# Kernel optimization log

Hardware: AMD Instinct MI355X
Metric: run time of the kernel (lower is better)

Reference implementation:

```python
import jax, jax.numpy as jnp
import numpy as np
from jax import lax

B, C, H, W = 2, 256, 64, 64
OUT_C = 256
D_QK = C // 16   # 16
D_V = C // 2     # 128
BN_EPS = 1e-5


def setup_inputs() -> dict:
    key = jax.random.key(0)
    ks = jax.random.split(key, 10)
    s = lambda fan: 1.0 / np.sqrt(fan)
    return {
        "input1": jax.random.normal(ks[0], (B, C, H, W), jnp.float32),
        "input2": jax.random.normal(ks[1], (B, C, H, W), jnp.float32),
        "Wq": jax.random.normal(ks[2], (D_QK, C), jnp.float32) * s(C),
        "bq": jnp.zeros((D_QK,), jnp.float32),
        "Wk": jax.random.normal(ks[3], (D_QK, C), jnp.float32) * s(C),
        "bk": jnp.zeros((D_QK,), jnp.float32),
        "Wv": jax.random.normal(ks[4], (D_V, C), jnp.float32) * s(C),
        "bv": jnp.zeros((D_V,), jnp.float32),
        "gamma": jnp.array(0.5, jnp.float32),  # nn.Parameter(zeros(1)); nonzero to exercise the path
        "Wcat": jax.random.normal(ks[5], (OUT_C, C, 3, 3), jnp.float32) * s(C * 9),
        "bn_gamma": jnp.ones((OUT_C,), jnp.float32),
        "bn_beta": jnp.zeros((OUT_C,), jnp.float32),
    }


def _conv1x1(x, Wt, b):
    # x: (B,C,H,W), Wt: (O,C) -> (B,O,H,W)
    return jnp.einsum('bchw,oc->bohw', x, Wt) + b[None, :, None, None]


def _branch(x_self, x_other, Wq, bq, Wk, bk, Wv, bv, gamma):
    N = H * W
    q = _conv1x1(x_self, Wq, bq).reshape(B, D_QK, N)   # q of self
    k = _conv1x1(x_other, Wk, bk).reshape(B, D_QK, N)  # k of other
    v = _conv1x1(x_self, Wv, bv).reshape(B, D_V, N)    # v of self
    # attn[b,n,m] = softmax_m( q[:,n] . k[:,m] / sqrt(d) )
    attn = jax.nn.softmax(jnp.einsum('bdn,bdm->bnm', q, k) / jnp.sqrt(jnp.float32(D_QK)), axis=-1)
    out = jnp.einsum('bcm,bnm->bcn', v, attn).reshape(B, D_V, H, W)  # v @ attn^T
    out = jnp.concatenate([out, x_self[:, :C // 2]], axis=1)  # (B,C,H,W)
    return gamma * out + x_self


def reference(input1, input2, Wq, bq, Wk, bk, Wv, bv, gamma, Wcat, bn_gamma, bn_beta):
    out1 = _branch(input1, input2, Wq, bq, Wk, bk, Wv, bv, gamma)
    out2 = _branch(input2, input1, Wq, bq, Wk, bk, Wv, bv, gamma)
    s = out1 + out2
    y = lax.conv_general_dilated(s, Wcat, (1, 1), 'SAME',
                                 dimension_numbers=('NCHW', 'OIHW', 'NCHW'))
    # BatchNorm (inference: running_mean=0, running_var=1)
    inv = 1.0 / jnp.sqrt(1.0 + BN_EPS)
    y = y * (bn_gamma * inv)[None, :, None, None] + bn_beta[None, :, None, None]
    feat_sum = jax.nn.relu(y)
    return (feat_sum, out1, out2)
```

## Files before the change

kernel.cpp:

```cpp
#include <hip/hip_runtime.h>

#define N_PIX 4096
#define CCH 256
#define DV 128

typedef __attribute__((ext_vector_type(8))) short bf16x8;
typedef __attribute__((ext_vector_type(4))) float f32x4;
typedef __attribute__((ext_vector_type(8))) short short8;

__device__ __forceinline__ short f2bf(float f) {
    unsigned u = __builtin_bit_cast(unsigned, f);
    u += 0x7fffu + ((u >> 16) & 1u);
    return (short)(u >> 16);
}

__global__ __launch_bounds__(512) void qkv_kernel(
    const float* __restrict__ x1, const float* __restrict__ x2,
    const short* __restrict__ wqkv,
    const float* __restrict__ bq, const float* __restrict__ bk,
    const float* __restrict__ bv,
    short* __restrict__ qb, short* __restrict__ kb, short* __restrict__ vb)
{
    __shared__ short xT[64][68];

    const int tid = threadIdx.x;
    const int lane = tid & 63;
    const int w = tid >> 6;
    const int g = lane >> 4, l15 = lane & 15;
    const int n0 = blockIdx.x * 64;
    const int ib = blockIdx.y;
    const int i = ib >> 1, b = ib & 1;
    const float* x = (i == 0 ? x1 : x2) + (size_t)b * CCH * N_PIX;

    const int px2 = tid & 31, c4 = tid >> 5;

    const int rhalf = (w >> 2) * 80;

    f32x4 acc[5];
    #pragma unroll
    for (int jl = 0; jl < 5; ++jl) {
        int rbase = rhalf + jl * 16;
        float bias;
        if (rbase == 0)       bias = bq[l15];
        else if (rbase == 16) bias = bk[l15];
        else                  bias = bv[rbase - 32 + l15];
        acc[jl] = (f32x4){bias, bias, bias, bias};
    }

    float2 xr[4];
    {
        #pragma unroll
        for (int jj = 0; jj < 4; ++jj)
            xr[jj] = *(const float2*)&x[(size_t)(c4 * 4 + jj) * N_PIX + n0 + px2 * 2];
    }

    for (int ci = 0; ci < 4; ++ci) {
        __syncthreads();
        {
            short4 w0, w1;
            w0.x = f2bf(xr[0].x); w0.y = f2bf(xr[1].x); w0.z = f2bf(xr[2].x); w0.w = f2bf(xr[3].x);
            w1.x = f2bf(xr[0].y); w1.y = f2bf(xr[1].y); w1.z = f2bf(xr[2].y); w1.w = f2bf(xr[3].y);
            *(short4*)&xT[px2 * 2 + 0][c4 * 4] = w0;
            *(short4*)&xT[px2 * 2 + 1][c4 * 4] = w1;
        }
        __syncthreads();
        if (ci < 3) {
            #pragma unroll
            for (int jj = 0; jj < 4; ++jj)
                xr[jj] = *(const float2*)
                    &x[(size_t)((ci + 1) * 64 + c4 * 4 + jj) * N_PIX + n0 + px2 * 2];
        }
        bf16x8 a0 = *(const bf16x8*)&xT[(w & 3) * 16 + l15][g * 8];
        bf16x8 a1 = *(const bf16x8*)&xT[(w & 3) * 16 + l15][32 + g * 8];
        #pragma unroll
        for (int jl = 0; jl < 5; ++jl) {
            int rbase = rhalf + jl * 16;
            const short* wrow = wqkv + (size_t)(rbase + l15) * CCH + ci * 64;
            bf16x8 b0 = *(const bf16x8*)&wrow[g * 8];
            bf16x8 b1 = *(const bf16x8*)&wrow[32 + g * 8];
            acc[jl] = __builtin_amdgcn_mfma_f32_16x16x32_bf16(a0, b0, acc[jl], 0, 0, 0);
            acc[jl] = __builtin_amdgcn_mfma_f32_16x16x32_bf16(a1, b1, acc[jl], 0, 0, 0);
        }
    }

    const int px_base = n0 + (w & 3) * 16 + g * 4;
    #pragma unroll
    for (int jl = 0; jl < 5; ++jl) {
        int rbase = rhalf + jl * 16;
        if (rbase == 0) {
            #pragma unroll
            for (int rr = 0; rr < 4; ++rr)
                qb[((size_t)ib * N_PIX + px_base + rr) * 16 + l15] = f2bf(acc[jl][rr]);
        } else if (rbase == 16) {
            #pragma unroll
            for (int rr = 0; rr < 4; ++rr)
                kb[((size_t)ib * N_PIX + px_base + rr) * 16 + l15] = f2bf(acc[jl][rr]);
        } else {
            int c = rbase - 32 + l15;
            short4 s;
            s.x = f2bf(acc[jl][0]); s.y = f2bf(acc[jl][1]);
            s.z = f2bf(acc[jl][2]); s.w = f2bf(acc[jl][3]);
            *(short4*)&vb[((size_t)ib * DV + c) * N_PIX + px_base] = s;
        }
    }
}

__global__ __launch_bounds__(256, 4) void attn_kernel(
    const short* __restrict__ qg, const short* __restrict__ kg,
    const short* __restrict__ vg,
    float* __restrict__ out1, float* __restrict__ out2,
    float* __restrict__ featf, float* __restrict__ lpart)
{
    __shared__ short k_lds[64 * 24];
    __shared__ short p_lds[64 * 72];

    const int tid = threadIdx.x;
    const int lane = tid & 63;
    const int w = tid >> 6;
    const int gk = lane >> 4;
    const int l15 = lane & 15;

    const int B_ = blockIdx.x;
    const int pm = B_ & 7;
    const int pb = pm >> 1, mh = pm & 1;
    const int nt = B_ >> 3;
    const int n0 = nt * 64;
    const int br = pb >> 1, b = pb & 1;

    const short* qp = qg + (size_t)pb * N_PIX * 16;
    const short* kp = kg + (size_t)((br ^ 1) * 2 + b) * N_PIX * 16 + (size_t)(mh * 2048) * 16;
    const short* vp = vg + (size_t)pb * DV * N_PIX + mh * 2048;

    bf16x8 aq = {};
    if (lane < 32)
        aq = *(const bf16x8*)&qp[(size_t)(n0 + w * 16 + l15) * 16 + gk * 8];

    f32x4 acc[2][4];
    #pragma unroll
    for (int cc = 0; cc < 2; ++cc)
        #pragma unroll
        for (int nb = 0; nb < 4; ++nb) acc[cc][nb] = (f32x4){0.f, 0.f, 0.f, 0.f};
    float lsum[4] = {0.f, 0.f, 0.f, 0.f};

    const short* vbase = vp + (size_t)(w * 32 + l15) * N_PIX + gk * 8;
    const int krow = tid - 192;

    int4 vbuf0[4], vbuf1[4];
    int4 kr0 = {}, kr1 = {};

    {
        #pragma unroll
        for (int cc = 0; cc < 2; ++cc)
            #pragma unroll
            for (int m2 = 0; m2 < 2; ++m2)
                vbuf0[cc * 2 + m2] = *(const int4*)&vbase[(size_t)cc * 16 * N_PIX + m2 * 32];
        if (tid >= 192) {
            kr0 = *(const int4*)&kp[(size_t)krow * 16];
            kr1 = *(const int4*)&kp[(size_t)krow * 16 + 8];
            *(int4*)&k_lds[krow * 24] = kr0;
            *(int4*)&k_lds[krow * 24 + 8] = kr1;
        }
        __syncthreads();
    }

    for (int t0 = 0; t0 < 32; t0 += 2) {
        #pragma unroll
        for (int half = 0; half < 2; ++half) {
            const int t = t0 + half;
            int4* vcur = half ? vbuf1 : vbuf0;
            int4* vnxt = half ? vbuf0 : vbuf1;
            if (t + 1 < 32) {
                #pragma unroll
                for (int cc = 0; cc < 2; ++cc)
                    #pragma unroll
                    for (int m2 = 0; m2 < 2; ++m2)
                        vnxt[cc * 2 + m2] = *(const int4*)
                            &vbase[(size_t)cc * 16 * N_PIX + (t + 1) * 64 + m2 * 32];
                if (tid >= 192) {
                    kr0 = *(const int4*)&kp[(size_t)((t + 1) * 64 + krow) * 16];
                    kr1 = *(const int4*)&kp[(size_t)((t + 1) * 64 + krow) * 16 + 8];
                }
            }
            #pragma unroll
            for (int h = 0; h < 4; ++h) {
                bf16x8 bk_ = {};
                if (lane < 32)
                    bk_ = *(const bf16x8*)&k_lds[(h * 16 + l15) * 24 + gk * 8];
                f32x4 s = __builtin_amdgcn_mfma_f32_16x16x32_bf16(
                    aq, bk_, (f32x4){0.f, 0.f, 0.f, 0.f}, 0, 0, 0);
                #pragma unroll
                for (int rr = 0; rr < 4; ++rr) {
                    float e = __expf(s[rr] * 0.25f);
                    lsum[rr] += e;
                    unsigned u = __builtin_bit_cast(unsigned, e);
                    p_lds[(w * 16 + gk * 4 + rr) * 72 + h * 16 + l15] = (short)(u >> 16);
                }
            }
            __syncthreads();
            if (t + 1 < 32 && tid >= 192) {
                *(int4*)&k_lds[krow * 24] = kr0;
                *(int4*)&k_lds[krow * 24 + 8] = kr1;
            }
            __builtin_amdgcn_s_setprio(1);
            #pragma unroll
            for (int m2 = 0; m2 < 2; ++m2) {
                #pragma unroll
                for (int nb = 0; nb < 4; ++nb) {
                    bf16x8 bp = *(const bf16x8*)&p_lds[(nb * 16 + l15) * 72 + m2 * 32 + gk * 8];
                    #pragma unroll
                    for (int cc = 0; cc < 2; ++cc) {
                        bf16x8 av = __builtin_bit_cast(bf16x8, vcur[cc * 2 + m2]);
                        acc[cc][nb] = __builtin_amdgcn_mfma_f32_16x16x32_bf16(
                            av, bp, acc[cc][nb], 0, 0, 0);
                    }
                }
            }
            __builtin_amdgcn_s_setprio(0);
            __syncthreads();
        }
    }

    #pragma unroll
    for (int rr = 0; rr < 4; ++rr) {
        float v = lsum[rr];
        v += __shfl_xor(v, 1); v += __shfl_xor(v, 2);
        v += __shfl_xor(v, 4); v += __shfl_xor(v, 8);
        lsum[rr] = v;
    }
    if (l15 == 0) {
        #pragma unroll
        for (int rr = 0; rr < 4; ++rr)
            lpart[(size_t)(pb * 2 + mh) * N_PIX + n0 + w * 16 + gk * 4 + rr] = lsum[rr];
    }

    if (mh == 0) {
        float* Od = (br ? out2 : out1) + (size_t)b * CCH * N_PIX;
        #pragma unroll
        for (int cc = 0; cc < 2; ++cc)
            #pragma unroll
            for (int nb = 0; nb < 4; ++nb)
                #pragma unroll
                for (int rr = 0; rr < 4; ++rr) {
                    int c = w * 32 + cc * 16 + gk * 4 + rr;
                    Od[(size_t)c * N_PIX + n0 + nb * 16 + l15] = acc[cc][nb][rr];
                }
    } else {
        float* Ps = featf + (size_t)(pb * 64 + nt) * (128 * 64);
        #pragma unroll
        for (int cc = 0; cc < 2; ++cc)
            #pragma unroll
            for (int nb = 0; nb < 4; ++nb)
                #pragma unroll
                for (int rr = 0; rr < 4; ++rr) {
                    int c = w * 32 + cc * 16 + gk * 4 + rr;
                    Ps[c * 64 + nb * 16 + l15] = acc[cc][nb][rr];
                }
    }
}

__global__ __launch_bounds__(256) void merge_kernel(
    const float* __restrict__ x1, const float* __restrict__ x2,
    const float* __restrict__ featf, const float* __restrict__ lpart,
    const float* __restrict__ gamma_p,
    float* __restrict__ out1, float* __restrict__ out2,
    short* __restrict__ s_t)
{
    __shared__ short st[32 * 264];
    __shared__ float rls[2][32];
    const int tid = threadIdx.x;
    const int px0 = blockIdx.x * 32;
    const int b = blockIdx.y;
    const int nt = blockIdx.x >> 1;
    const int q32 = (blockIdx.x & 1) * 32;
    const float* xa_ = x1 + (size_t)b * CCH * N_PIX;
    const float* xb_ = x2 + (size_t)b * CCH * N_PIX;
    float* o1 = out1 + (size_t)b * CCH * N_PIX;
    float* o2 = out2 + (size_t)b * CCH * N_PIX;
    const float* T1 = featf + (size_t)(b * 64 + nt) * (128 * 64);
    const float* T2 = featf + (size_t)((2 + b) * 64 + nt) * (128 * 64);

    if (tid < 64) {
        int h = tid >> 5, j = tid & 31;
        int pbh = h ? (2 + b) : b;
        float l = lpart[(size_t)(pbh * 2 + 0) * N_PIX + px0 + j]
                + lpart[(size_t)(pbh * 2 + 1) * N_PIX + px0 + j];
        rls[h][j] = 1.0f / l;
    }
    __syncthreads();
    const float gmm = gamma_p[0];

    for (int idx = tid; idx < 2048; idx += 256) {
        int c = idx >> 3, p4 = idx & 7;
        size_t off = (size_t)c * N_PIX + px0 + p4 * 4;
        float4 va = *(const float4*)&xa_[off];
        float4 vb2 = *(const float4*)&xb_[off];
        float4 r1, r2;
        if (c < 128) {
            float4 pa = *(const float4*)&o1[off];
            float4 pc = *(const float4*)&o2[off];
            float4 a1 = *(const float4*)&T1[c * 64 + q32 + p4 * 4];
            float4 c1 = *(const float4*)&T2[c * 64 + q32 + p4 * 4];
            r1.x = gmm * (pa.x + a1.x) * rls[0][p4 * 4 + 0] + va.x;
            r1.y = gmm * (pa.y + a1.y) * rls[0][p4 * 4 + 1] + va.y;
            r1.z = gmm * (pa.z + a1.z) * rls[0][p4 * 4 + 2] + va.z;
            r1.w = gmm * (pa.w + a1.w) * rls[0][p4 * 4 + 3] + va.w;
            r2.x = gmm * (pc.x + c1.x) * rls[1][p4 * 4 + 0] + vb2.x;
            r2.y = gmm * (pc.y + c1.y) * rls[1][p4 * 4 + 1] + vb2.y;
            r2.z = gmm * (pc.z + c1.z) * rls[1][p4 * 4 + 2] + vb2.z;
            r2.w = gmm * (pc.w + c1.w) * rls[1][p4 * 4 + 3] + vb2.w;
        } else {
            size_t offl = (size_t)(c - 128) * N_PIX + px0 + p4 * 4;
            float4 val = *(const float4*)&xa_[offl];
            float4 vbl = *(const float4*)&xb_[offl];
            r1.x = gmm * val.x + va.x; r1.y = gmm * val.y + va.y;
            r1.z = gmm * val.z + va.z; r1.w = gmm * val.w + va.w;
            r2.x = gmm * vbl.x + vb2.x; r2.y = gmm * vbl.y + vb2.y;
            r2.z = gmm * vbl.z + vb2.z; r2.w = gmm * vbl.w + vb2.w;
        }
        *(float4*)&o1[off] = r1;
        *(float4*)&o2[off] = r2;
        st[(p4 * 4 + 0) * 264 + c] = f2bf(r1.x + r2.x);
        st[(p4 * 4 + 1) * 264 + c] = f2bf(r1.y + r2.y);
        st[(p4 * 4 + 2) * 264 + c] = f2bf(r1.z + r2.z);
        st[(p4 * 4 + 3) * 264 + c] = f2bf(r1.w + r2.w);
    }
    __syncthreads();
    for (int idx = tid; idx < 1024; idx += 256) {
        int px = idx >> 5, seg = idx & 31;
        int4 v = *(const int4*)&st[px * 264 + seg * 8];
        *(int4*)&s_t[((size_t)b * N_PIX + px0 + px) * CCH + seg * 8] = v;
    }
}

__global__ __launch_bounds__(256) void prep_w(
    const float* __restrict__ Wcat,
    const float* __restrict__ Wq, const float* __restrict__ Wk,
    const float* __restrict__ Wv,
    short* __restrict__ wfmt, short* __restrict__ wqkv)
{
    if (blockIdx.x < 288) {
        int idx = blockIdx.x * 256 + threadIdx.x;
        int lane = idx & 63;
        int ocg = (idx >> 6) & 15;
        int chunk = (idx >> 10) & 7;
        int tap = idx >> 13;
        int oc = ocg * 16 + (lane & 15);
        int ic0 = chunk * 32 + (lane >> 4) * 8;
        short8 v;
        #pragma unroll
        for (int j = 0; j < 8; ++j)
            v[j] = f2bf(Wcat[((size_t)oc * CCH + ic0 + j) * 9 + tap]);
        *(short8*)&wfmt[(size_t)idx * 8] = v;
    } else {
        int idx = (blockIdx.x - 288) * 1024 + threadIdx.x * 4;
        int r = idx >> 8, c = idx & 255;
        const float* src;
        if (r < 16)      src = Wq + (size_t)r * CCH + c;
        else if (r < 32) src = Wk + (size_t)(r - 16) * CCH + c;
        else             src = Wv + (size_t)(r - 32) * CCH + c;
        float4 f = *(const float4*)src;
        short4 s;
        s.x = f2bf(f.x); s.y = f2bf(f.y); s.z = f2bf(f.z); s.w = f2bf(f.w);
        *(short4*)&wqkv[idx] = s;
    }
}

__global__ __launch_bounds__(256) void conv_mfma(
    const short* __restrict__ s_t, const short* __restrict__ wfmt,
    const float* __restrict__ bn_gamma, const float* __restrict__ bn_beta,
    float* __restrict__ feat)
{
    __shared__ short s_lds[264 * 40];
    const int tid = threadIdx.x;
    const int lane = tid & 63;
    const int wv = tid >> 6;
    const int g = lane >> 4, l15 = lane & 15;

    const int bx = blockIdx.x;
    const int oc_t = bx & 3;
    const int pt = bx >> 2;
    const int b = pt >> 5;
    const int h0 = (pt & 31) * 2;

    f32x4 acc[2][4] = {};

    const short* sbase = s_t + (size_t)b * N_PIX * CCH;
    const short* wf = wfmt + ((size_t)(oc_t * 4) * 64 + lane) * 8;

    for (int ci = 0; ci < 8; ++ci) {
        const int ic0 = ci * 32;
        __syncthreads();
        for (int idx = tid; idx < 1056; idx += 256) {
            int seg = idx & 3, pos = idx >> 2;
            int row = pos / 66, wi = pos - row * 66;
            int hr = h0 - 1 + row, w = wi - 1;
            int4 val = {0, 0, 0, 0};
            if (hr >= 0 && hr < 64 && (unsigned)w < 64u)
                val = *(const int4*)&sbase[((size_t)(hr * 64 + w)) * CCH + ic0 + seg * 8];
            *(int4*)&s_lds[pos * 40 + seg * 8] = val;
        }
        __syncthreads();

        const short* wfc = wf + (size_t)ci * 8192;
        bf16x8 a0[4], a1[4];
        #pragma unroll
        for (int j = 0; j < 4; ++j) a0[j] = *(const bf16x8*)&wfc[j * 512];

        for (int tap = 0; tap < 9; ++tap) {
            bf16x8* ac = (tap & 1) ? a1 : a0;
            bf16x8* an = (tap & 1) ? a0 : a1;
            if (tap < 8) {
                const short* wfn = wfc + (size_t)(tap + 1) * 65536;
                #pragma unroll
                for (int j = 0; j < 4; ++j) an[j] = *(const bf16x8*)&wfn[j * 512];
            }
            int ky = (tap >= 6) ? 2 : (tap >= 3 ? 1 : 0);
            int kx = tap - ky * 3;
            #pragma unroll
            for (int f = 0; f < 2; ++f) {
                int fr = wv * 2 + f;
                int rl = fr >> 2, wc0 = (fr & 3) * 16;
                bf16x8 bb = *(const bf16x8*)
                    &s_lds[((rl + ky) * 66 + wc0 + l15 + kx) * 40 + g * 8];
                #pragma unroll
                for (int j = 0; j < 4; ++j)
                    acc[f][j] = __builtin_amdgcn_mfma_f32_16x16x32_bf16(
                        ac[j], bb, acc[f][j], 0, 0, 0);
            }
        }
    }

    const float inv = rsqrtf(1.0f + 1e-5f);
    #pragma unroll
    for (int f = 0; f < 2; ++f) {
        int fr = wv * 2 + f;
        int rl = fr >> 2, wc0 = (fr & 3) * 16;
        int h = h0 + rl, wcol = wc0 + l15;
        #pragma unroll
        for (int j = 0; j < 4; ++j) {
            #pragma unroll
            for (int r = 0; r < 4; ++r) {
                int oc = oc_t * 64 + j * 16 + g * 4 + r;
                float y = acc[f][j][r] * (bn_gamma[oc] * inv) + bn_beta[oc];
                feat[((size_t)b * CCH + oc) * N_PIX + h * 64 + wcol] = fmaxf(y, 0.f);
            }
        }
    }
}

extern "C" void kernel_launch(void* const* d_in, const int* in_sizes, int n_in,
                              void* d_out, int out_size, void* d_ws, size_t ws_size,
                              hipStream_t stream) {
    const float* x1    = (const float*)d_in[0];
    const float* x2    = (const float*)d_in[1];
    const float* Wq    = (const float*)d_in[2];
    const float* bq    = (const float*)d_in[3];
    const float* Wk    = (const float*)d_in[4];
    const float* bk    = (const float*)d_in[5];
    const float* Wv    = (const float*)d_in[6];
    const float* bv    = (const float*)d_in[7];
    const float* gamma = (const float*)d_in[8];
    const float* Wcat  = (const float*)d_in[9];
    const float* bng   = (const float*)d_in[10];
    const float* bnb   = (const float*)d_in[11];

    float* out  = (float*)d_out;
    float* feat = out;
    float* out1 = out + 2097152;
    float* out2 = out + 4194304;

    short* ws   = (short*)d_ws;
    short* qb   = ws;
    short* kb   = ws + 262144;
    short* vb   = ws + 524288;
    short* s_t  = ws + 2621440;
    short* wfmt = ws + 4718592;
    float* lp   = (float*)(ws + 5308416);
    short* wqkv = s_t;

    prep_w<<<328, 256, 0, stream>>>(Wcat, Wq, Wk, Wv, wfmt, wqkv);
    qkv_kernel<<<dim3(64, 4), 512, 0, stream>>>(x1, x2, wqkv, bq, bk, bv, qb, kb, vb);
    attn_kernel<<<512, 256, 0, stream>>>(qb, kb, vb, out1, out2, feat, lp);
    merge_kernel<<<dim3(128, 2), 256, 0, stream>>>(x1, x2, feat, lp, gamma, out1, out2, s_t);
    conv_mfma<<<256, 256, 0, stream>>>(s_t, wfmt, bng, bnb, feat);
}
```

Before: 109.1 us.

## Split attention keys three ways, store bf16 partials, and use single-row conv tiles

The attention kernel now splits the key range into three chunks instead of two, giving 768 blocks for better occupancy. The two non-primary partial outputs are packed to bf16 through LDS and written with coalesced int4 stores, halving partial-buffer traffic. The merge kernel now sums three partial denominators and two bf16 partial numerators. The conv kernel processes one output row per block with 512 blocks and launch bounds of 2. Trade-off: bf16 partials lose precision, and the uneven split leaves the last chunk shorter.

```diff
diff --git a/kernel.cpp b/kernel.cpp
--- a/kernel.cpp
+++ b/kernel.cpp
@@ -12,6 +12,16 @@
     unsigned u = __builtin_bit_cast(unsigned, f);
     u += 0x7fffu + ((u >> 16) & 1u);
     return (short)(u >> 16);
+}
+
+__device__ __forceinline__ float4 bf4_load(const short* p) {
+    short4 s = *(const short4*)p;
+    float4 f;
+    f.x = __builtin_bit_cast(float, (unsigned)((unsigned short)s.x) << 16);
+    f.y = __builtin_bit_cast(float, (unsigned)((unsigned short)s.y) << 16);
+    f.z = __builtin_bit_cast(float, (unsigned)((unsigned short)s.z) << 16);
+    f.w = __builtin_bit_cast(float, (unsigned)((unsigned short)s.w) << 16);
+    return f;
 }
 
 __global__ __launch_bounds__(512) void qkv_kernel(
@@ -33,7 +43,6 @@
     const float* x = (i == 0 ? x1 : x2) + (size_t)b * CCH * N_PIX;
 
     const int px2 = tid & 31, c4 = tid >> 5;
-
     const int rhalf = (w >> 2) * 80;
 
     f32x4 acc[5];
@@ -109,7 +118,7 @@
     const short* __restrict__ qg, const short* __restrict__ kg,
     const short* __restrict__ vg,
     float* __restrict__ out1, float* __restrict__ out2,
-    float* __restrict__ featf, float* __restrict__ lpart)
+    short* __restrict__ featp, float* __restrict__ lpart)
 {
     __shared__ short k_lds[64 * 24];
     __shared__ short p_lds[64 * 72];
@@ -121,15 +130,17 @@
     const int l15 = lane & 15;
 
     const int B_ = blockIdx.x;
-    const int pm = B_ & 7;
-    const int pb = pm >> 1, mh = pm & 1;
-    const int nt = B_ >> 3;
+    const int pb = B_ & 3;
+    const int mh = (B_ >> 2) % 3;
+    const int nt = B_ / 12;
     const int n0 = nt * 64;
     const int br = pb >> 1, b = pb & 1;
+    const int tstart = mh * 22;
+    const int tend = (mh == 2) ? 64 : tstart + 22;
 
     const short* qp = qg + (size_t)pb * N_PIX * 16;
-    const short* kp = kg + (size_t)((br ^ 1) * 2 + b) * N_PIX * 16 + (size_t)(mh * 2048) * 16;
-    const short* vp = vg + (size_t)pb * DV * N_PIX + mh * 2048;
+    const short* kp = kg + (size_t)((br ^ 1) * 2 + b) * N_PIX * 16;
+    const short* vp = vg + (size_t)pb * DV * N_PIX;
 
     bf16x8 aq = {};
     if (lane < 32)
@@ -153,23 +164,24 @@
         for (int cc = 0; cc < 2; ++cc)
             #pragma unroll
             for (int m2 = 0; m2 < 2; ++m2)
-                vbuf0[cc * 2 + m2] = *(const int4*)&vbase[(size_t)cc * 16 * N_PIX + m2 * 32];
+                vbuf0[cc * 2 + m2] = *(const int4*)
+                    &vbase[(size_t)cc * 16 * N_PIX + tstart * 64 + m2 * 32];
         if (tid >= 192) {
-            kr0 = *(const int4*)&kp[(size_t)krow * 16];
-            kr1 = *(const int4*)&kp[(size_t)krow * 16 + 8];
+            kr0 = *(const int4*)&kp[(size_t)(tstart * 64 + krow) * 16];
+            kr1 = *(const int4*)&kp[(size_t)(tstart * 64 + krow) * 16 + 8];
             *(int4*)&k_lds[krow * 24] = kr0;
             *(int4*)&k_lds[krow * 24 + 8] = kr1;
         }
         __syncthreads();
     }
 
-    for (int t0 = 0; t0 < 32; t0 += 2) {
+    for (int t0 = tstart; t0 < tend; t0 += 2) {
         #pragma unroll
         for (int half = 0; half < 2; ++half) {
             const int t = t0 + half;
             int4* vcur = half ? vbuf1 : vbuf0;
             int4* vnxt = half ? vbuf0 : vbuf1;
-            if (t + 1 < 32) {
+            if (t + 1 < tend) {
                 #pragma unroll
                 for (int cc = 0; cc < 2; ++cc)
                     #pragma unroll
@@ -197,7 +209,7 @@
                 }
             }
             __syncthreads();
-            if (t + 1 < 32 && tid >= 192) {
+            if (t + 1 < tend && tid >= 192) {
                 *(int4*)&k_lds[krow * 24] = kr0;
                 *(int4*)&k_lds[krow * 24 + 8] = kr1;
             }
@@ -230,7 +242,7 @@
     if (l15 == 0) {
         #pragma unroll
         for (int rr = 0; rr < 4; ++rr)
-            lpart[(size_t)(pb * 2 + mh) * N_PIX + n0 + w * 16 + gk * 4 + rr] = lsum[rr];
+            lpart[(size_t)(pb * 3 + mh) * N_PIX + n0 + w * 16 + gk * 4 + rr] = lsum[rr];
     }
 
     if (mh == 0) {
@@ -245,22 +257,36 @@
                     Od[(size_t)c * N_PIX + n0 + nb * 16 + l15] = acc[cc][nb][rr];
                 }
     } else {
-        float* Ps = featf + (size_t)(pb * 64 + nt) * (128 * 64);
-        #pragma unroll
-        for (int cc = 0; cc < 2; ++cc)
-            #pragma unroll
-            for (int nb = 0; nb < 4; ++nb)
+        short* Ps = featp + (size_t)(pb * 2 + (mh - 1)) * (64 * 128 * 64)
+                          + (size_t)nt * (128 * 64);
+        #pragma unroll
+        for (int chalf = 0; chalf < 2; ++chalf) {
+            if ((w >> 1) == chalf) {
+                int crel_base = (w & 1) * 32;
                 #pragma unroll
-                for (int rr = 0; rr < 4; ++rr) {
-                    int c = w * 32 + cc * 16 + gk * 4 + rr;
-                    Ps[c * 64 + nb * 16 + l15] = acc[cc][nb][rr];
-                }
+                for (int cc = 0; cc < 2; ++cc)
+                    #pragma unroll
+                    for (int nb = 0; nb < 4; ++nb)
+                        #pragma unroll
+                        for (int rr = 0; rr < 4; ++rr) {
+                            int crel = crel_base + cc * 16 + gk * 4 + rr;
+                            p_lds[crel * 66 + nb * 16 + l15] = f2bf(acc[cc][nb][rr]);
+                        }
+            }
+            __syncthreads();
+            for (int idx = tid; idx < 512; idx += 256) {
+                int cr = idx >> 3, seg = idx & 7;
+                int4 v = *(const int4*)&p_lds[cr * 66 + seg * 8];
+                *(int4*)&Ps[(size_t)(chalf * 64 + cr) * 64 + seg * 8] = v;
+            }
+            __syncthreads();
+        }
     }
 }
 
 __global__ __launch_bounds__(256) void merge_kernel(
     const float* __restrict__ x1, const float* __restrict__ x2,
-    const float* __restrict__ featf, const float* __restrict__ lpart,
+    const short* __restrict__ featp, const float* __restrict__ lpart,
     const float* __restrict__ gamma_p,
     float* __restrict__ out1, float* __restrict__ out2,
     short* __restrict__ s_t)
@@ -276,14 +302,17 @@
     const float* xb_ = x2 + (size_t)b * CCH * N_PIX;
     float* o1 = out1 + (size_t)b * CCH * N_PIX;
     float* o2 = out2 + (size_t)b * CCH * N_PIX;
-    const float* T1 = featf + (size_t)(b * 64 + nt) * (128 * 64);
-    const float* T2 = featf + (size_t)((2 + b) * 64 + nt) * (128 * 64);
+    const short* T10 = featp + (size_t)(b * 2 + 0) * (64 * 128 * 64) + (size_t)nt * (128 * 64);
+    const short* T11 = featp + (size_t)(b * 2 + 1) * (64 * 128 * 64) + (size_t)nt * (128 * 64);
+    const short* T20 = featp + (size_t)((2 + b) * 2 + 0) * (64 * 128 * 64) + (size_t)nt * (128 * 64);
+    const short* T21 = featp + (size_t)((2 + b) * 2 + 1) * (64 * 128 * 64) + (size_t)nt * (128 * 64);
 
     if (tid < 64) {
         int h = tid >> 5, j = tid & 31;
         int pbh = h ? (2 + b) : b;
-        float l = lpart[(size_t)(pbh * 2 + 0) * N_PIX + px0 + j]
-                + lpart[(size_t)(pbh * 2 + 1) * N_PIX + px0 + j];
+        float l = lpart[(size_t)(pbh * 3 + 0) * N_PIX + px0 + j]
+                + lpart[(size_t)(pbh * 3 + 1) * N_PIX + px0 + j]
+                + lpart[(size_t)(pbh * 3 + 2) * N_PIX + px0 + j];
         rls[h][j] = 1.0f / l;
     }
     __syncthreads();
@@ -296,18 +325,21 @@
         float4 vb2 = *(const float4*)&xb_[off];
         float4 r1, r2;
         if (c < 128) {
+            int toff = c * 64 + q32 + p4 * 4;
             float4 pa = *(const float4*)&o1[off];
             float4 pc = *(const float4*)&o2[off];
-            float4 a1 = *(const float4*)&T1[c * 64 + q32 + p4 * 4];
-            float4 c1 = *(const float4*)&T2[c * 64 + q32 + p4 * 4];
-            r1.x = gmm * (pa.x + a1.x) * rls[0][p4 * 4 + 0] + va.x;
-            r1.y = gmm * (pa.y + a1.y) * rls[0][p4 * 4 + 1] + va.y;
-            r1.z = gmm * (pa.z + a1.z) * rls[0][p4 * 4 + 2] + va.z;
-            r1.w = gmm * (pa.w + a1.w) * rls[0][p4 * 4 + 3] + va.w;
-            r2.x = gmm * (pc.x + c1.x) * rls[1][p4 * 4 + 0] + vb2.x;
-            r2.y = gmm * (pc.y + c1.y) * rls[1][p4 * 4 + 1] + vb2.y;
-            r2.z = gmm * (pc.z + c1.z) * rls[1][p4 * 4 + 2] + vb2.z;
-            r2.w = gmm * (pc.w + c1.w) * rls[1][p4 * 4 + 3] + vb2.w;
+            float4 a1 = bf4_load(&T10[toff]);
+            float4 a2 = bf4_load(&T11[toff]);
+            float4 c1 = bf4_load(&T20[toff]);
+            float4 c2 = bf4_load(&T21[toff]);
+            r1.x = gmm * (pa.x + a1.x + a2.x) * rls[0][p4 * 4 + 0] + va.x;
+            r1.y = gmm * (pa.y + a1.y + a2.y) * rls[0][p4 * 4 + 1] + va.y;
+            r1.z = gmm * (pa.z + a1.z + a2.z) * rls[0][p4 * 4 + 2] + va.z;
+            r1.w = gmm * (pa.w + a1.w + a2.w) * rls[0][p4 * 4 + 3] + va.w;
+            r2.x = gmm * (pc.x + c1.x + c2.x) * rls[1][p4 * 4 + 0] + vb2.x;
+            r2.y = gmm * (pc.y + c1.y + c2.y) * rls[1][p4 * 4 + 1] + vb2.y;
+            r2.z = gmm * (pc.z + c1.z + c2.z) * rls[1][p4 * 4 + 2] + vb2.z;
+            r2.w = gmm * (pc.w + c1.w + c2.w) * rls[1][p4 * 4 + 3] + vb2.w;
         } else {
             size_t offl = (size_t)(c - 128) * N_PIX + px0 + p4 * 4;
             float4 val = *(const float4*)&xa_[offl];
@@ -365,12 +397,12 @@
     }
 }
 
-__global__ __launch_bounds__(256) void conv_mfma(
+__global__ __launch_bounds__(256, 2) void conv_mfma(
     const short* __restrict__ s_t, const short* __restrict__ wfmt,
     const float* __restrict__ bn_gamma, const float* __restrict__ bn_beta,
     float* __restrict__ feat)
 {
-    __shared__ short s_lds[264 * 40];
+    __shared__ short s_lds[198 * 40];
     const int tid = threadIdx.x;
     const int lane = tid & 63;
     const int wv = tid >> 6;
@@ -379,10 +411,10 @@
     const int bx = blockIdx.x;
     const int oc_t = bx & 3;
     const int pt = bx >> 2;
-    const int b = pt >> 5;
-    const int h0 = (pt & 31) * 2;
-
-    f32x4 acc[2][4] = {};
+    const int b = pt >> 6;
+    const int h0 = pt & 63;
+
+    f32x4 acc[4] = {};
 
     const short* sbase = s_t + (size_t)b * N_PIX * CCH;
     const short* wf = wfmt + ((size_t)(oc_t * 4) * 64 + lane) * 8;
@@ -390,7 +422,7 @@
     for (int ci = 0; ci < 8; ++ci) {
         const int ic0 = ci * 32;
         __syncthreads();
-        for (int idx = tid; idx < 1056; idx += 256) {
+        for (int idx = tid; idx < 792; idx += 256) {
             int seg = idx & 3, pos = idx >> 2;
             int row = pos / 66, wi = pos - row * 66;
             int hr = h0 - 1 + row, w = wi - 1;
@@ -416,34 +448,24 @@
             }
             int ky = (tap >= 6) ? 2 : (tap >= 3 ? 1 : 0);
             int kx = tap - ky * 3;
-            #pragma unroll
-            for (int f = 0; f < 2; ++f) {
-                int fr = wv * 2 + f;
-                int rl = fr >> 2, wc0 = (fr & 3) * 16;
-                bf16x8 bb = *(const bf16x8*)
-                    &s_lds[((rl + ky) * 66 + wc0 + l15 + kx) * 40 + g * 8];
-                #pragma unroll
-                for (int j = 0; j < 4; ++j)
-                    acc[f][j] = __builtin_amdgcn_mfma_f32_16x16x32_bf16(
-                        ac[j], bb, acc[f][j], 0, 0, 0);
-            }
+            bf16x8 bb = *(const bf16x8*)
+                &s_lds[(ky * 66 + wv * 16 + l15 + kx) * 40 + g * 8];
+            #pragma unroll
+            for (int j = 0; j < 4; ++j)
+                acc[j] = __builtin_amdgcn_mfma_f32_16x16x32_bf16(
+                    ac[j], bb, acc[j], 0, 0, 0);
         }
     }
 
     const float inv = rsqrtf(1.0f + 1e-5f);
+    const int wcol = wv * 16 + l15;
     #pragma unroll
-    for (int f = 0; f < 2; ++f) {
-        int fr = wv * 2 + f;
-        int rl = fr >> 2, wc0 = (fr & 3) * 16;
-        int h = h0 + rl, wcol = wc0 + l15;
-        #pragma unroll
-        for (int j = 0; j < 4; ++j) {
-            #pragma unroll
-            for (int r = 0; r < 4; ++r) {
-                int oc = oc_t * 64 + j * 16 + g * 4 + r;
-                float y = acc[f][j][r] * (bn_gamma[oc] * inv) + bn_beta[oc];
-                feat[((size_t)b * CCH + oc) * N_PIX + h * 64 + wcol] = fmaxf(y, 0.f);
-            }
+    for (int j = 0; j < 4; ++j) {
+        #pragma unroll
+        for (int r = 0; r < 4; ++r) {
+            int oc = oc_t * 64 + j * 16 + g * 4 + r;
+            float y = acc[j][r] * (bn_gamma[oc] * inv) + bn_beta[oc];
+            feat[((size_t)b * CCH + oc) * N_PIX + h0 * 64 + wcol] = fmaxf(y, 0.f);
         }
     }
 }
@@ -480,7 +502,7 @@
 
     prep_w<<<328, 256, 0, stream>>>(Wcat, Wq, Wk, Wv, wfmt, wqkv);
     qkv_kernel<<<dim3(64, 4), 512, 0, stream>>>(x1, x2, wqkv, bq, bk, bv, qb, kb, vb);
-    attn_kernel<<<512, 256, 0, stream>>>(qb, kb, vb, out1, out2, feat, lp);
-    merge_kernel<<<dim3(128, 2), 256, 0, stream>>>(x1, x2, feat, lp, gamma, out1, out2, s_t);
-    conv_mfma<<<256, 256, 0, stream>>>(s_t, wfmt, bng, bnb, feat);
-}
+    attn_kernel<<<768, 256, 0, stream>>>(qb, kb, vb, out1, out2, (short*)feat, lp);
+    merge_kernel<<<dim3(128, 2), 256, 0, stream>>>(x1, x2, (const short*)feat, lp, gamma, out1, out2, s_t);
+    conv_mfma<<<512, 256, 0, stream>>>(s_t, wfmt, bng, bnb, feat);
+}
```

Measured after the change: 107.1 us, median of 2. Within noise of the previous version (-1.8%).
